# Performance work log

Measured on AMD Instinct MI355X. Metric: run time of the kernel, lower is better.

Reference implementation:

```python
import jax, jax.numpy as jnp
import numpy as np

# config (matches init_kwargs)
NA, NEN = 8, 8            # n_agents, n_enemies
NENT = NA + NEN           # n_entities
NFA, NFE = 64, 64         # state_nf_al, state_nf_en
E, A, M, HE = 64, 64, 32, 64  # entity_embed, attn_embed, mixing_embed, hypernet_embed
TD, TE = 64, 64           # task_repre_dim, task_repre_embed_dim
BS, SL = 64, 512


def setup_inputs() -> dict:
    key = jax.random.key(0)
    ks = iter(jax.random.split(key, 32))
    def rn(shape, scale=0.05):
        return jax.random.normal(next(ks), shape, dtype=jnp.float32) * scale
    return {
        "agent_qs": rn((BS, SL, NA), 1.0),
        "states": rn((BS, SL, NA * NFA + NEN * NFE), 1.0),
        "task_repre_mu": rn((BS, SL, NA, TD), 1.0),
        "ally_w": rn((NFA, E)), "ally_b": rn((E,)),
        "enemy_w": rn((NFE, E)), "enemy_b": rn((E,)),
        "q_w": rn((E, A)), "q_b": rn((A,)),
        "k_w": rn((E, A)), "k_b": rn((A,)),
        "hw1_w1": rn((E + NFA + TE, HE)), "hw1_b1": rn((HE,)),
        "hw1_w2": rn((HE, M)), "hw1_b2": rn((M,)),
        "hwf_w1": rn((E + TE, HE)), "hwf_b1": rn((HE,)),
        "hwf_w2": rn((HE, M)), "hwf_b2": rn((M,)),
        "hb1_w": rn((E + TE, M)), "hb1_b": rn((M,)),
        "v_w1": rn((E + TE, M)), "v_b1": rn((M,)),
        "v_w2": rn((M, 1)), "v_b2": rn((1,)),
        "tre_w": rn((TD, TE)), "tre_b": rn((TE,)),
    }


def reference(agent_qs, states, task_repre_mu,
              ally_w, ally_b, enemy_w, enemy_b,
              q_w, q_b, k_w, k_b,
              hw1_w1, hw1_b1, hw1_w2, hw1_b2,
              hwf_w1, hwf_b1, hwf_w2, hwf_b2,
              hb1_w, hb1_b, v_w1, v_b1, v_w2, v_b2,
              tre_w, tre_b):
    bs, sl = agent_qs.shape[:2]
    # decompose_state (state_last_action=False, state_timestep_number=False)
    ally = states[..., : NA * NFA].reshape(bs, sl, NA, NFA)      # [bs,sl,NA,NFA]
    enemy = states[..., NA * NFA:].reshape(bs, sl, NEN, NFE)     # [bs,sl,NEN,NFE]
    ally_e = ally @ ally_w + ally_b                              # [bs,sl,NA,E]
    enemy_e = enemy @ enemy_w + enemy_b                          # [bs,sl,NEN,E]
    ent = jnp.concatenate([ally_e, enemy_e], axis=2)             # [bs,sl,NENT,E]
    q = ent @ q_w + q_b                                          # [bs,sl,NENT,A]
    k = ent @ k_w + k_b
    energy = jnp.einsum('bsqa,bska->bsqk', q, k)                 # [bs,sl,NENT,NENT]
    # torch: F.softmax(energy, dim=1) on [B,n_ent,n_ent] -> softmax over query axis
    attn = jax.nn.softmax(energy, axis=2)
    # attn_out = bmm(value[B,E,n], attn[B,n,n]).mean(-1)
    attn_out = jnp.einsum('bsne,bsnk->bse', ent, attn) / NENT    # [bs,sl,E]

    mean_mu = task_repre_mu.mean(axis=-2)                        # [bs,sl,TD]
    tre = task_repre_mu @ tre_w + tre_b                          # [bs,sl,NA,TE]
    mean_tre = mean_mu @ tre_w + tre_b                           # [bs,sl,TE]

    ent_mix = jnp.concatenate([
        jnp.broadcast_to(attn_out[:, :, None, :], (bs, sl, NA, E)),
        ally, tre], axis=-1)                                     # [bs,sl,NA,E+NFA+TE]
    mix = jnp.concatenate([attn_out, mean_tre], axis=-1)         # [bs,sl,E+TE]

    w1 = jnp.abs(jax.nn.relu(ent_mix @ hw1_w1 + hw1_b1) @ hw1_w2 + hw1_b2)  # [bs,sl,NA,M]
    b1 = mix @ hb1_w + hb1_b                                     # [bs,sl,M]
    hidden = jax.nn.elu(jnp.einsum('bsn,bsnm->bsm', agent_qs, w1) + b1)     # [bs,sl,M]
    wf = jnp.abs(jax.nn.relu(mix @ hwf_w1 + hwf_b1) @ hwf_w2 + hwf_b2)      # [bs,sl,M]
    v = jax.nn.relu(mix @ v_w1 + v_b1) @ v_w2 + v_b2             # [bs,sl,1]
    q_tot = jnp.einsum('bsm,bsm->bs', hidden, wf)[..., None] + v # [bs,sl,1]
    return q_tot
```

## Files before the change

### kernel.cpp

```cpp
#include <hip/hip_runtime.h>
#include <math.h>


#define TOKS 32768

typedef __attribute__((ext_vector_type(8))) short short8;
typedef __attribute__((ext_vector_type(4))) float f32x4;

#define MFMA(a, b, c) __builtin_amdgcn_mfma_f32_16x16x32_bf16((a), (b), (c), 0, 0, 0)

#define E_CAT   0
#define E_WQKT  8192
#define E_ZBRT  13312
#define E_H1T   29696
#define E_W2T   41984
#define E_WFT   44032
#define E_BF16_TOTAL 46080
#define E_AO_US 46464

__device__ __forceinline__ unsigned short bfr(float x) {
    unsigned u = __builtin_bit_cast(unsigned, x);
    u += 0x7fffu + ((u >> 16) & 1u);
    return (unsigned short)(u >> 16);
}
__device__ __forceinline__ float bf2f(unsigned short h) {
    unsigned u = ((unsigned)h) << 16;
    return __builtin_bit_cast(float, u);
}
__device__ __forceinline__ short8 cvt8v(float4 a, float4 b) {
    short8 r;
    r[0] = (short)bfr(a.x); r[1] = (short)bfr(a.y);
    r[2] = (short)bfr(a.z); r[3] = (short)bfr(a.w);
    r[4] = (short)bfr(b.x); r[5] = (short)bfr(b.y);
    r[6] = (short)bfr(b.z); r[7] = (short)bfr(b.w);
    return r;
}
#define SWZ64(r, c)  ((((r) * 64)  + (c)) ^ (((r) & 7) << 3))
#define SWZ128(r, c) ((((r) * 128) + (c)) ^ (((r) & 7) << 3))
#define SWZ192(r, c) ((((r) * 192) + (c)) ^ (((r) & 7) << 3))

__global__ __launch_bounds__(256) void qmix_setup(
    const float* __restrict__ ally_w, const float* __restrict__ enemy_w,
    const float* __restrict__ q_w, const float* __restrict__ k_w,
    const float* __restrict__ k_b,
    const float* __restrict__ hw1_w1, const float* __restrict__ hw1_b1,
    const float* __restrict__ hw1_w2,
    const float* __restrict__ hwf_w1, const float* __restrict__ hwf_b1,
    const float* __restrict__ hwf_w2,
    const float* __restrict__ hb1_w, const float* __restrict__ hb1_b,
    const float* __restrict__ v_w1, const float* __restrict__ v_b1,
    const float* __restrict__ tre_w, const float* __restrict__ tre_b,
    unsigned short* __restrict__ wsb, float* __restrict__ wsf)
{
    int gid = blockIdx.x * 256 + threadIdx.x;
    if (gid < E_BF16_TOTAL) {
        float v = 0.f;
        int base, r, c, K;
        if (gid < E_WQKT) {
            base = E_CAT; K = 128;
            int i = gid - base; r = i >> 7; c = i & 127;
            v = (c < 64) ? ally_w[c * 64 + r] : enemy_w[(c - 64) * 64 + r];
        } else if (gid < E_ZBRT) {
            base = E_WQKT; K = 64;
            int i = gid - base; r = i >> 6; c = i & 63;
            if (r < 64) {
                for (int g = 0; g < 64; ++g) v += q_w[c * 64 + g] * k_w[r * 64 + g];
            } else if (r == 64) {
                for (int g = 0; g < 64; ++g) v += q_w[c * 64 + g] * k_b[g];
            }
        } else if (gid < E_H1T) {
            base = E_ZBRT; K = 128;
            int i = gid - base; r = i >> 7; c = i & 127;
            if (r < 64) {
                if (c < 64) v = hwf_w1[c * 64 + r];
                else for (int g = 0; g < 64; ++g) v += tre_w[(c - 64) * 64 + g] * hwf_w1[(64 + g) * 64 + r];
            } else if (r < 96) {
                int m = r - 64;
                if (c < 64) v = hb1_w[c * 32 + m];
                else for (int g = 0; g < 64; ++g) v += tre_w[(c - 64) * 64 + g] * hb1_w[(64 + g) * 32 + m];
            } else {
                int m = r - 96;
                if (c < 64) v = v_w1[c * 32 + m];
                else for (int g = 0; g < 64; ++g) v += tre_w[(c - 64) * 64 + g] * v_w1[(64 + g) * 32 + m];
            }
        } else if (gid < E_W2T) {
            base = E_H1T; K = 192;
            int i = gid - base; r = i / 192; c = i % 192;
            if (c < 64) v = hw1_w1[(64 + c) * 64 + r];
            else if (c < 128) {
                for (int g = 0; g < 64; ++g) v += tre_w[(c - 64) * 64 + g] * hw1_w1[(128 + g) * 64 + r];
            } else v = hw1_w1[(c - 128) * 64 + r];
        } else if (gid < E_WFT) {
            base = E_W2T; K = 64;
            int i = gid - base; r = i >> 6; c = i & 63;
            v = hw1_w2[c * 32 + r];
        } else {
            base = E_WFT; K = 64;
            int i = gid - base; r = i >> 6; c = i & 63;
            v = hwf_w2[c * 32 + r];
        }
        wsb[base + ((r * K + c) ^ ((r & 7) << 3))] = bfr(v);
    } else if (gid < E_BF16_TOTAL + 192) {
        int j = gid - E_BF16_TOTAL; float v;
        if (j < 64) {
            v = hw1_b1[j];
            for (int g = 0; g < 64; ++g) v += tre_b[g] * hw1_w1[(128 + g) * 64 + j];
        } else if (j < 128) {
            int e = j - 64; v = hwf_b1[e];
            for (int g = 0; g < 64; ++g) v += tre_b[g] * hwf_w1[(64 + g) * 64 + e];
        } else if (j < 160) {
            int m = j - 128; v = hb1_b[m];
            for (int g = 0; g < 64; ++g) v += tre_b[g] * hb1_w[(64 + g) * 32 + m];
        } else {
            int m = j - 160; v = v_b1[m];
            for (int g = 0; g < 64; ++g) v += tre_b[g] * v_w1[(64 + g) * 32 + m];
        }
        wsf[j] = v;
    }
}

__global__ __launch_bounds__(512) void qmix_attn(
    const float* __restrict__ states,
    const float* __restrict__ ally_b, const float* __restrict__ enemy_b,
    const unsigned short* __restrict__ wsb,
    unsigned short* __restrict__ aoG)
{
    __shared__ unsigned short sWa[13312];
    __shared__ unsigned short sE[8][1024];
    __shared__ unsigned short sT[8][1024];

    const int lane = threadIdx.x & 63;
    const int wv   = threadIdx.x >> 6;
    const int l15  = lane & 15;
    const int lg   = lane >> 4;
    const int kb   = lg * 8;
    const int tok0 = blockIdx.x * 32;

    const short8 zero8 = {0, 0, 0, 0, 0, 0, 0, 0};
    const f32x4  zero4 = {0.f, 0.f, 0.f, 0.f};

    for (int i = threadIdx.x * 8; i < 13312; i += 512 * 8)
        *(short8*)(sWa + i) = *(const short8*)(wsb + E_CAT + i);
    __syncthreads();
    const unsigned short* lCAT  = sWa;
    const unsigned short* lWQKT = sWa + 8192;

    unsigned short* E = sE[wv];
    unsigned short* T = sT[wv];

    const int roff = (l15 < 8) ? (l15 * 64 + kb) : (512 + (l15 - 8) * 64 + kb);
    float4 pf[4];
    {
        const float* p = states + (size_t)(tok0 + wv * 4) * 1024 + roff;
        pf[0] = *(const float4*)(p);      pf[1] = *(const float4*)(p + 4);
        pf[2] = *(const float4*)(p + 32); pf[3] = *(const float4*)(p + 36);
    }

    for (int ti = 0; ti < 4; ++ti) {
        const size_t t = (size_t)(tok0 + wv * 4 + ti);
        float4 cur0 = pf[0], cur1 = pf[1], cur2 = pf[2], cur3 = pf[3];
        if (ti < 3) {
            const float* p = states + (t + 1) * 1024 + roff;
            pf[0] = *(const float4*)(p);      pf[1] = *(const float4*)(p + 4);
            pf[2] = *(const float4*)(p + 32); pf[3] = *(const float4*)(p + 36);
        }
        short8 a01 = cvt8v(cur0, cur1);
        short8 a23 = cvt8v(cur2, cur3);
        const bool isally = (l15 < 8);

        f32x4 accB[4] = {zero4, zero4, zero4, zero4};
        #pragma unroll
        for (int ks = 0; ks < 4; ++ks) {
            short8 af;
            if (ks == 0)      af = isally ? a01 : zero8;
            else if (ks == 1) af = isally ? a23 : zero8;
            else if (ks == 2) af = isally ? zero8 : a01;
            else              af = isally ? zero8 : a23;
            #pragma unroll
            for (int nt = 0; nt < 4; ++nt) {
                short8 w = *(const short8*)&lCAT[SWZ128(nt * 16 + l15, ks * 32 + kb)];
                accB[nt] = MFMA(af, w, accB[nt]);
            }
        }
        #pragma unroll
        for (int nt = 0; nt < 4; ++nt) {
            int col = nt * 16 + l15;
            float ab = ally_b[col], eb = enemy_b[col];
            #pragma unroll
            for (int reg = 0; reg < 4; ++reg) {
                int r = lg * 4 + reg;
                E[SWZ64(r, col)] = bfr(accB[nt][reg] + (r < 8 ? ab : eb));
            }
        }

        f32x4 accC[5] = {zero4, zero4, zero4, zero4, zero4};
        #pragma unroll
        for (int ks = 0; ks < 2; ++ks) {
            short8 ef = *(const short8*)&E[SWZ64(l15, ks * 32 + kb)];
            #pragma unroll
            for (int nt = 0; nt < 5; ++nt) {
                short8 w = *(const short8*)&lWQKT[SWZ64(nt * 16 + l15, ks * 32 + kb)];
                accC[nt] = MFMA(ef, w, accC[nt]);
            }
        }
        const int src = lane & 48;
        float si[4];
        #pragma unroll
        for (int reg = 0; reg < 4; ++reg) si[reg] = __shfl(accC[4][reg], src);
        #pragma unroll
        for (int nt = 0; nt < 4; ++nt)
            #pragma unroll
            for (int reg = 0; reg < 4; ++reg)
                T[SWZ64(lg * 4 + reg, nt * 16 + l15)] = bfr(accC[nt][reg]);

        f32x4 en = zero4;
        #pragma unroll
        for (int ks = 0; ks < 2; ++ks) {
            short8 ta = *(const short8*)&T[SWZ64(l15, ks * 32 + kb)];
            short8 ba = *(const short8*)&E[SWZ64(l15, ks * 32 + kb)];
            en = MFMA(ta, ba, en);
        }
        #pragma unroll
        for (int reg = 0; reg < 4; ++reg) en[reg] += si[reg];

        float mx = fmaxf(fmaxf(en[0], en[1]), fmaxf(en[2], en[3]));
        mx = fmaxf(mx, __shfl_xor(mx, 16));
        mx = fmaxf(mx, __shfl_xor(mx, 32));
        float p0 = __expf(en[0] - mx), p1 = __expf(en[1] - mx);
        float p2 = __expf(en[2] - mx), p3 = __expf(en[3] - mx);
        float s = p0 + p1 + p2 + p3;
        s += __shfl_xor(s, 16);
        s += __shfl_xor(s, 32);
        float inv = 1.f / s;
        float r0 = p0 * inv, r1 = p1 * inv, r2 = p2 * inv, r3 = p3 * inv;
        r0 += __shfl_xor(r0, 1); r0 += __shfl_xor(r0, 2); r0 += __shfl_xor(r0, 4); r0 += __shfl_xor(r0, 8);
        r1 += __shfl_xor(r1, 1); r1 += __shfl_xor(r1, 2); r1 += __shfl_xor(r1, 4); r1 += __shfl_xor(r1, 8);
        r2 += __shfl_xor(r2, 1); r2 += __shfl_xor(r2, 2); r2 += __shfl_xor(r2, 4); r2 += __shfl_xor(r2, 8);
        r3 += __shfl_xor(r3, 1); r3 += __shfl_xor(r3, 2); r3 += __shfl_xor(r3, 4); r3 += __shfl_xor(r3, 8);
        float rr[4] = {r0, r1, r2, r3};
        float ao = 0.f;
        #pragma unroll
        for (int reg = 0; reg < 4; ++reg) {
            ao += rr[reg] * bf2f(E[SWZ64(lg * 4 + reg, lane)]);
            float ra = __shfl_xor(rr[reg], 16);
            float rb = __shfl_xor(rr[reg], 32);
            float rc = __shfl_xor(rr[reg], 48);
            ao += ra * bf2f(E[SWZ64((lg ^ 1) * 4 + reg, lane)]);
            ao += rb * bf2f(E[SWZ64((lg ^ 2) * 4 + reg, lane)]);
            ao += rc * bf2f(E[SWZ64((lg ^ 3) * 4 + reg, lane)]);
        }
        aoG[t * 64 + lane] = bfr(ao * 0.0625f);
    }
}

__device__ __forceinline__ short8 mmfrag(const float* __restrict__ mp) {
    float a0 = 0.f, a1 = 0.f, a2 = 0.f, a3 = 0.f, a4 = 0.f, a5 = 0.f, a6 = 0.f, a7 = 0.f;
    #pragma unroll
    for (int a = 0; a < 8; ++a) {
        float4 u = *(const float4*)(mp + a * 64);
        float4 v = *(const float4*)(mp + a * 64 + 4);
        a0 += u.x; a1 += u.y; a2 += u.z; a3 += u.w;
        a4 += v.x; a5 += v.y; a6 += v.z; a7 += v.w;
    }
    return cvt8v(make_float4(a0 * 0.125f, a1 * 0.125f, a2 * 0.125f, a3 * 0.125f),
                 make_float4(a4 * 0.125f, a5 * 0.125f, a6 * 0.125f, a7 * 0.125f));
}

__global__ __launch_bounds__(256) void qmix_hyper(
    const float* __restrict__ agent_qs, const float* __restrict__ states,
    const float* __restrict__ mu,
    const float* __restrict__ v_w2, const float* __restrict__ v_b2,
    const float* __restrict__ hw1_b2, const float* __restrict__ hwf_b2,
    const unsigned short* __restrict__ wsb, const float* __restrict__ wsf,
    const unsigned short* __restrict__ aoG,
    float* __restrict__ out)
{
    __shared__ unsigned short sWb[16384];
    __shared__ unsigned short sZ[4][1024];
    __shared__ unsigned short sH1[4][2048];
    __shared__ float sB1[4][512];
    __shared__ float sWF[4][512];
    __shared__ float sV[4][16];

    const int lane = threadIdx.x & 63;
    const int wv   = threadIdx.x >> 6;
    const int l15  = lane & 15;
    const int lg   = lane >> 4;
    const int kb   = lg * 8;
    const int T0   = blockIdx.x * 64 + wv * 16;

    const float* BHF = wsf + 64;
    const float* BB1 = wsf + 128;
    const float* BV  = wsf + 160;
    const float* BH1 = wsf + 0;

    const f32x4 zero4 = {0.f, 0.f, 0.f, 0.f};

    for (int i = threadIdx.x * 8; i < 16384; i += 256 * 8)
        *(short8*)(sWb + i) = *(const short8*)(wsb + E_ZBRT + i);
    __syncthreads();

    f32x4 zb[8] = {zero4, zero4, zero4, zero4, zero4, zero4, zero4, zero4};
    #pragma unroll
    for (int ks = 0; ks < 4; ++ks) {
        short8 af;
        if (ks < 2)
            af = *(const short8*)&aoG[(size_t)(T0 + l15) * 64 + ks * 32 + kb];
        else
            af = mmfrag(mu + (size_t)(T0 + l15) * 512 + (ks - 2) * 32 + kb);
        #pragma unroll
        for (int nt = 0; nt < 8; ++nt) {
            short8 w = *(const short8*)&sWb[SWZ128(nt * 16 + l15, ks * 32 + kb)];
            zb[nt] = MFMA(af, w, zb[nt]);
        }
    }
    __syncthreads();

    for (int i = threadIdx.x * 8; i < 16384; i += 256 * 8)
        *(short8*)(sWb + i) = *(const short8*)(wsb + E_H1T + i);

    #pragma unroll
    for (int nt = 0; nt < 4; ++nt) {
        int col = nt * 16 + l15;
        float bz = BHF[col];
        #pragma unroll
        for (int reg = 0; reg < 4; ++reg)
            sZ[wv][SWZ64(lg * 4 + reg, col)] = bfr(fmaxf(zb[nt][reg] + bz, 0.f));
    }
    #pragma unroll
    for (int nt = 4; nt < 6; ++nt) {
        int m = (nt - 4) * 16 + l15;
        float bb = BB1[m];
        #pragma unroll
        for (int reg = 0; reg < 4; ++reg)
            sB1[wv][(lg * 4 + reg) * 32 + m] = zb[nt][reg] + bb;
    }
    {
        float bv0 = BV[l15], bv1 = BV[16 + l15];
        float vw0 = v_w2[l15], vw1 = v_w2[16 + l15];
        #pragma unroll
        for (int reg = 0; reg < 4; ++reg) {
            float vp = fmaxf(zb[6][reg] + bv0, 0.f) * vw0
                     + fmaxf(zb[7][reg] + bv1, 0.f) * vw1;
            vp += __shfl_xor(vp, 1); vp += __shfl_xor(vp, 2);
            vp += __shfl_xor(vp, 4); vp += __shfl_xor(vp, 8);
            if (l15 == 0) sV[wv][lg * 4 + reg] = vp;
        }
    }
    __syncthreads();
    const unsigned short* lH1T = sWb;
    const unsigned short* lW2T = sWb + 12288;
    const unsigned short* lWFT = sWb + 14336;

    {
        f32x4 wfa = zero4, wfb = zero4;
        #pragma unroll
        for (int ks = 0; ks < 2; ++ks) {
            short8 af = *(const short8*)&sZ[wv][SWZ64(l15, ks * 32 + kb)];
            short8 b0 = *(const short8*)&lWFT[SWZ64(l15, ks * 32 + kb)];
            short8 b1 = *(const short8*)&lWFT[SWZ64(16 + l15, ks * 32 + kb)];
            wfa = MFMA(af, b0, wfa);
            wfb = MFMA(af, b1, wfb);
        }
        float hb0 = hwf_b2[l15], hb1 = hwf_b2[16 + l15];
        #pragma unroll
        for (int reg = 0; reg < 4; ++reg) {
            int tok = lg * 4 + reg;
            sWF[wv][tok * 32 + l15]      = fabsf(wfa[reg] + hb0);
            sWF[wv][tok * 32 + 16 + l15] = fabsf(wfb[reg] + hb1);
        }
    }

    const float vb2 = v_b2[0];
    const float b20 = hw1_b2[l15], b21 = hw1_b2[16 + l15];
    const int agent = l15 & 7;

    for (int c = 0; c < 4; ++c) {
        f32x4 h[2][4] = {{zero4, zero4, zero4, zero4}, {zero4, zero4, zero4, zero4}};
        #pragma unroll
        for (int ks = 0; ks < 6; ++ks) {
            #pragma unroll
            for (int ff = 0; ff < 2; ++ff) {
                const size_t tok = (size_t)(T0 + c * 4 + ff * 2 + (l15 >> 3));
                short8 af;
                if (ks < 2)
                    af = cvt8v(*(const float4*)(states + tok * 1024 + agent * 64 + ks * 32 + kb),
                               *(const float4*)(states + tok * 1024 + agent * 64 + ks * 32 + kb + 4));
                else if (ks < 4)
                    af = cvt8v(*(const float4*)(mu + tok * 512 + agent * 64 + (ks - 2) * 32 + kb),
                               *(const float4*)(mu + tok * 512 + agent * 64 + (ks - 2) * 32 + kb + 4));
                else
                    af = *(const short8*)&aoG[tok * 64 + (ks - 4) * 32 + kb];
                #pragma unroll
                for (int nt = 0; nt < 4; ++nt) {
                    short8 w = *(const short8*)&lH1T[SWZ192(nt * 16 + l15, ks * 32 + kb)];
                    h[ff][nt] = MFMA(af, w, h[ff][nt]);
                }
            }
        }
        #pragma unroll
        for (int ff = 0; ff < 2; ++ff)
            #pragma unroll
            for (int nt = 0; nt < 4; ++nt) {
                int col = nt * 16 + l15;
                float bh = BH1[col];
                #pragma unroll
                for (int reg = 0; reg < 4; ++reg)
                    sH1[wv][SWZ64(ff * 16 + lg * 4 + reg, col)] =
                        bfr(fmaxf(h[ff][nt][reg] + bh, 0.f));
            }

        f32x4 wa[2] = {zero4, zero4}, wb[2] = {zero4, zero4};
        #pragma unroll
        for (int ks = 0; ks < 2; ++ks) {
            short8 b0 = *(const short8*)&lW2T[SWZ64(l15, ks * 32 + kb)];
            short8 b1 = *(const short8*)&lW2T[SWZ64(16 + l15, ks * 32 + kb)];
            #pragma unroll
            for (int ff = 0; ff < 2; ++ff) {
                short8 af = *(const short8*)&sH1[wv][SWZ64(ff * 16 + l15, ks * 32 + kb)];
                wa[ff] = MFMA(af, b0, wa[ff]);
                wb[ff] = MFMA(af, b1, wb[ff]);
            }
        }

        #pragma unroll
        for (int ff = 0; ff < 2; ++ff) {
            const int tokL = c * 4 + ff * 2 + (lg >> 1);
            float hp0 = 0.f, hp1 = 0.f;
            #pragma unroll
            for (int reg = 0; reg < 4; ++reg) {
                float qsv = agent_qs[(size_t)(T0 + tokL) * 8 + (lg & 1) * 4 + reg];
                hp0 += qsv * fabsf(wa[ff][reg] + b20);
                hp1 += qsv * fabsf(wb[ff][reg] + b21);
            }
            hp0 += __shfl_xor(hp0, 16);
            hp1 += __shfl_xor(hp1, 16);
            float e0 = hp0 + sB1[wv][tokL * 32 + l15];
            float e1 = hp1 + sB1[wv][tokL * 32 + 16 + l15];
            float hid0 = e0 > 0.f ? e0 : (__expf(e0) - 1.f);
            float hid1 = e1 > 0.f ? e1 : (__expf(e1) - 1.f);
            float q = hid0 * sWF[wv][tokL * 32 + l15]
                    + hid1 * sWF[wv][tokL * 32 + 16 + l15];
            q += __shfl_xor(q, 1); q += __shfl_xor(q, 2);
            q += __shfl_xor(q, 4); q += __shfl_xor(q, 8);
            if (l15 == 0 && (lg & 1) == 0)
                out[T0 + tokL] = q + sV[wv][tokL] + vb2;
        }
    }
}

extern "C" void kernel_launch(void* const* d_in, const int* in_sizes, int n_in,
                              void* d_out, int out_size, void* d_ws, size_t ws_size,
                              hipStream_t stream)
{
    const float* agent_qs = (const float*)d_in[0];
    const float* states   = (const float*)d_in[1];
    const float* mu       = (const float*)d_in[2];
    const float* ally_w   = (const float*)d_in[3];
    const float* ally_b   = (const float*)d_in[4];
    const float* enemy_w  = (const float*)d_in[5];
    const float* enemy_b  = (const float*)d_in[6];
    const float* q_w      = (const float*)d_in[7];
    const float* k_w      = (const float*)d_in[9];
    const float* k_b      = (const float*)d_in[10];
    const float* hw1_w1   = (const float*)d_in[11];
    const float* hw1_b1   = (const float*)d_in[12];
    const float* hw1_w2   = (const float*)d_in[13];
    const float* hw1_b2   = (const float*)d_in[14];
    const float* hwf_w1   = (const float*)d_in[15];
    const float* hwf_b1   = (const float*)d_in[16];
    const float* hwf_w2   = (const float*)d_in[17];
    const float* hwf_b2   = (const float*)d_in[18];
    const float* hb1_w    = (const float*)d_in[19];
    const float* hb1_b    = (const float*)d_in[20];
    const float* v_w1     = (const float*)d_in[21];
    const float* v_b1     = (const float*)d_in[22];
    const float* v_w2     = (const float*)d_in[23];
    const float* v_b2     = (const float*)d_in[24];
    const float* tre_w    = (const float*)d_in[25];
    const float* tre_b    = (const float*)d_in[26];

    unsigned short* wsb = (unsigned short*)d_ws;
    float* wsf = (float*)((char*)d_ws + (size_t)E_BF16_TOTAL * 2);
    unsigned short* aoG = wsb + E_AO_US;
    float* out = (float*)d_out;

    hipLaunchKernelGGL(qmix_setup, dim3(181), dim3(256), 0, stream,
                       ally_w, enemy_w, q_w, k_w, k_b,
                       hw1_w1, hw1_b1, hw1_w2,
                       hwf_w1, hwf_b1, hwf_w2,
                       hb1_w, hb1_b, v_w1, v_b1, tre_w, tre_b,
                       wsb, wsf);

    hipLaunchKernelGGL(qmix_attn, dim3(TOKS / 32), dim3(512), 0, stream,
                       states, ally_b, enemy_b, wsb, aoG);

    hipLaunchKernelGGL(qmix_hyper, dim3(TOKS / 64), dim3(256), 0, stream,
                       agent_qs, states, mu, v_w2, v_b2, hw1_b2, hwf_b2,
                       wsb, wsf, aoG, out);
}
```

Before: 97.98 us.

## Precompose entity embedding with fused query-key weight to remove a serial GEMM stage

A new setup kernel folds the ally/enemy embedding weights and biases into the combined query-key transform, so the attention kernel computes both the entity embedding and the transformed query in one MFMA pass straight from the raw state features. The per-entity scalar bias term is now computed in fp32 from the raw features with a dot product and shuffles. This removes the dependent second GEMM and its LDS round trip. In exchange it adds a small kernel launch, doubles the MFMA work in the first stage, and uses more shared memory for the extra weight tile. Rounding also changes because the composed weights are quantized to bf16 once.

```diff
diff --git a/kernel.cpp b/kernel.cpp
--- a/kernel.cpp
+++ b/kernel.cpp
@@ -17,6 +17,8 @@
 #define E_WFT   44032
 #define E_BF16_TOTAL 46080
 #define E_AO_US 46464
+#define E_CATQ  2143616
+#define WSF2_BYTE 4303616
 
 __device__ __forceinline__ unsigned short bfr(float x) {
     unsigned u = __builtin_bit_cast(unsigned, x);
@@ -119,13 +121,54 @@
     }
 }
 
+__global__ __launch_bounds__(256) void qmix_setup2(
+    const float* __restrict__ ally_w, const float* __restrict__ enemy_w,
+    const float* __restrict__ ally_b, const float* __restrict__ enemy_b,
+    unsigned short* __restrict__ wsb, float* __restrict__ wsf2)
+{
+    int gid = blockIdx.x * 256 + threadIdx.x;
+    if (gid < 8192) {
+        int n = gid >> 7, k = gid & 127;
+        const float* wp = (k < 64) ? &ally_w[k * 64] : &enemy_w[(k - 64) * 64];
+        float v = 0.f;
+        for (int g = 0; g < 64; ++g)
+            v += wp[g] * bf2f(wsb[E_WQKT + SWZ64(n, g)]);
+        wsb[E_CATQ + SWZ128(n, k)] = bfr(v);
+    } else if (gid < 8192 + 128) {
+        int k = gid - 8192;
+        const float* wp = (k < 64) ? &ally_w[k * 64] : &enemy_w[(k - 64) * 64];
+        float v = 0.f;
+        for (int g = 0; g < 64; ++g)
+            v += wp[g] * bf2f(wsb[E_WQKT + SWZ64(64, g)]);
+        wsf2[k] = v;
+    } else if (gid < 8192 + 256) {
+        int j = gid - 8192 - 128;
+        int n = j & 63;
+        const float* bp = (j < 64) ? ally_b : enemy_b;
+        float v = 0.f;
+        for (int e = 0; e < 64; ++e)
+            v += bp[e] * bf2f(wsb[E_WQKT + SWZ64(n, e)]);
+        wsf2[128 + j] = v;
+    } else if (gid == 8192 + 256) {
+        float v = 0.f;
+        for (int e = 0; e < 64; ++e)
+            v += ally_b[e] * bf2f(wsb[E_WQKT + SWZ64(64, e)]);
+        wsf2[256] = v;
+    } else if (gid == 8192 + 257) {
+        float v = 0.f;
+        for (int e = 0; e < 64; ++e)
+            v += enemy_b[e] * bf2f(wsb[E_WQKT + SWZ64(64, e)]);
+        wsf2[257] = v;
+    }
+}
+
 __global__ __launch_bounds__(512) void qmix_attn(
     const float* __restrict__ states,
     const float* __restrict__ ally_b, const float* __restrict__ enemy_b,
-    const unsigned short* __restrict__ wsb,
+    const unsigned short* __restrict__ wsb, const float* __restrict__ wsf2,
     unsigned short* __restrict__ aoG)
 {
-    __shared__ unsigned short sWa[13312];
+    __shared__ unsigned short sWa[16384];
     __shared__ unsigned short sE[8][1024];
     __shared__ unsigned short sT[8][1024];
 
@@ -139,14 +182,30 @@
     const short8 zero8 = {0, 0, 0, 0, 0, 0, 0, 0};
     const f32x4  zero4 = {0.f, 0.f, 0.f, 0.f};
 
-    for (int i = threadIdx.x * 8; i < 13312; i += 512 * 8)
-        *(short8*)(sWa + i) = *(const short8*)(wsb + E_CAT + i);
+    for (int i = threadIdx.x * 8; i < 8192; i += 512 * 8) {
+        *(short8*)(sWa + i)        = *(const short8*)(wsb + E_CAT + i);
+        *(short8*)(sWa + 8192 + i) = *(const short8*)(wsb + E_CATQ + i);
+    }
     __syncthreads();
     const unsigned short* lCAT  = sWa;
-    const unsigned short* lWQKT = sWa + 8192;
+    const unsigned short* lCATQ = sWa + 8192;
 
     unsigned short* E = sE[wv];
     unsigned short* T = sT[wv];
+
+    const int off = (l15 < 8) ? 0 : 64;
+    float4 u2v0 = *(const float4*)(wsf2 + off + kb);
+    float4 u2v1 = *(const float4*)(wsf2 + off + kb + 4);
+    float4 u2v2 = *(const float4*)(wsf2 + off + 32 + kb);
+    float4 u2v3 = *(const float4*)(wsf2 + off + 32 + kb + 4);
+    const float csel = (l15 < 8) ? wsf2[256] : wsf2[257];
+    float tsel[4], biasEnt[4];
+    #pragma unroll
+    for (int nt = 0; nt < 4; ++nt) {
+        int col = nt * 16 + l15;
+        tsel[nt]    = wsf2[128 + (lg < 2 ? 0 : 64) + col];
+        biasEnt[nt] = (lg < 2) ? ally_b[col] : enemy_b[col];
+    }
 
     const int roff = (l15 < 8) ? (l15 * 64 + kb) : (512 + (l15 - 8) * 64 + kb);
     float4 pf[4];
@@ -168,7 +227,16 @@
         short8 a23 = cvt8v(cur2, cur3);
         const bool isally = (l15 < 8);
 
+        float si = cur0.x*u2v0.x + cur0.y*u2v0.y + cur0.z*u2v0.z + cur0.w*u2v0.w
+                 + cur1.x*u2v1.x + cur1.y*u2v1.y + cur1.z*u2v1.z + cur1.w*u2v1.w
+                 + cur2.x*u2v2.x + cur2.y*u2v2.y + cur2.z*u2v2.z + cur2.w*u2v2.w
+                 + cur3.x*u2v3.x + cur3.y*u2v3.y + cur3.z*u2v3.z + cur3.w*u2v3.w;
+        si += __shfl_xor(si, 16);
+        si += __shfl_xor(si, 32);
+        si += csel;
+
         f32x4 accB[4] = {zero4, zero4, zero4, zero4};
+        f32x4 accC[4] = {zero4, zero4, zero4, zero4};
         #pragma unroll
         for (int ks = 0; ks < 4; ++ks) {
             short8 af;
@@ -178,40 +246,21 @@
             else              af = isally ? zero8 : a23;
             #pragma unroll
             for (int nt = 0; nt < 4; ++nt) {
-                short8 w = *(const short8*)&lCAT[SWZ128(nt * 16 + l15, ks * 32 + kb)];
-                accB[nt] = MFMA(af, w, accB[nt]);
+                short8 w  = *(const short8*)&lCAT [SWZ128(nt * 16 + l15, ks * 32 + kb)];
+                short8 w2 = *(const short8*)&lCATQ[SWZ128(nt * 16 + l15, ks * 32 + kb)];
+                accB[nt] = MFMA(af, w,  accB[nt]);
+                accC[nt] = MFMA(af, w2, accC[nt]);
             }
         }
         #pragma unroll
         for (int nt = 0; nt < 4; ++nt) {
-            int col = nt * 16 + l15;
-            float ab = ally_b[col], eb = enemy_b[col];
             #pragma unroll
             for (int reg = 0; reg < 4; ++reg) {
                 int r = lg * 4 + reg;
-                E[SWZ64(r, col)] = bfr(accB[nt][reg] + (r < 8 ? ab : eb));
-            }
-        }
-
-        f32x4 accC[5] = {zero4, zero4, zero4, zero4, zero4};
-        #pragma unroll
-        for (int ks = 0; ks < 2; ++ks) {
-            short8 ef = *(const short8*)&E[SWZ64(l15, ks * 32 + kb)];
-            #pragma unroll
-            for (int nt = 0; nt < 5; ++nt) {
-                short8 w = *(const short8*)&lWQKT[SWZ64(nt * 16 + l15, ks * 32 + kb)];
-                accC[nt] = MFMA(ef, w, accC[nt]);
-            }
-        }
-        const int src = lane & 48;
-        float si[4];
-        #pragma unroll
-        for (int reg = 0; reg < 4; ++reg) si[reg] = __shfl(accC[4][reg], src);
-        #pragma unroll
-        for (int nt = 0; nt < 4; ++nt)
-            #pragma unroll
-            for (int reg = 0; reg < 4; ++reg)
-                T[SWZ64(lg * 4 + reg, nt * 16 + l15)] = bfr(accC[nt][reg]);
+                E[SWZ64(r, nt * 16 + l15)] = bfr(accB[nt][reg] + biasEnt[nt]);
+                T[SWZ64(r, nt * 16 + l15)] = bfr(accC[nt][reg] + tsel[nt]);
+            }
+        }
 
         f32x4 en = zero4;
         #pragma unroll
@@ -221,7 +270,8 @@
             en = MFMA(ta, ba, en);
         }
         #pragma unroll
-        for (int reg = 0; reg < 4; ++reg) en[reg] += si[reg];
+        for (int reg = 0; reg < 4; ++reg)
+            en[reg] += __shfl(si, lg * 4 + reg);
 
         float mx = fmaxf(fmaxf(en[0], en[1]), fmaxf(en[2], en[3]));
         mx = fmaxf(mx, __shfl_xor(mx, 16));
@@ -481,7 +531,8 @@
     const float* tre_b    = (const float*)d_in[26];
 
     unsigned short* wsb = (unsigned short*)d_ws;
-    float* wsf = (float*)((char*)d_ws + (size_t)E_BF16_TOTAL * 2);
+    float* wsf  = (float*)((char*)d_ws + (size_t)E_BF16_TOTAL * 2);
+    float* wsf2 = (float*)((char*)d_ws + (size_t)WSF2_BYTE);
     unsigned short* aoG = wsb + E_AO_US;
     float* out = (float*)d_out;
 
@@ -492,8 +543,11 @@
                        hb1_w, hb1_b, v_w1, v_b1, tre_w, tre_b,
                        wsb, wsf);
 
+    hipLaunchKernelGGL(qmix_setup2, dim3(34), dim3(256), 0, stream,
+                       ally_w, enemy_w, ally_b, enemy_b, wsb, wsf2);
+
     hipLaunchKernelGGL(qmix_attn, dim3(TOKS / 32), dim3(512), 0, stream,
-                       states, ally_b, enemy_b, wsb, aoG);
+                       states, ally_b, enemy_b, wsb, wsf2, aoG);
 
     hipLaunchKernelGGL(qmix_hyper, dim3(TOKS / 64), dim3(256), 0, stream,
                        agent_qs, states, mu, v_w2, v_b2, hw1_b2, hwf_b2,
```

Result: slower. 148.4 us (+51.4%).
